# Kernel tuning notes

Measured on AMD Instinct MI355X. Metric: run time of the kernel, lower is better.

## Reference

```python
import jax, jax.numpy as jnp
import numpy as np
import math

B, SEQ_IN, D_IN = 4, 1028, 64
D = 1024          # hidden_size
H = 16            # num_heads
HD = D // H       # head_dim
L = 4             # num_layers
D_OUT = 1
EPS = 1e-6


def setup_inputs() -> dict:
    key = jax.random.key(0)
    ks = iter(jax.random.split(key, 32))
    s = 0.02
    inp = {}
    inp['x'] = jax.random.normal(next(ks), (B, SEQ_IN, D_IN), jnp.float32)
    # conv frontend (torch Conv1d weight layout: [out_ch, in_ch, k])
    inp['conv1_w'] = jax.random.normal(next(ks), (D // 2, D_IN, 3), jnp.float32) * s
    inp['conv1_b'] = jnp.zeros((D // 2,), jnp.float32)
    inp['conv2_w'] = jax.random.normal(next(ks), (D, D // 2, 3), jnp.float32) * s
    inp['conv2_b'] = jnp.zeros((D,), jnp.float32)
    # stacked per-layer params [L, ...]
    inp['lnA_w'] = jnp.ones((L, D), jnp.float32)
    inp['lnA_b'] = jnp.zeros((L, D), jnp.float32)
    inp['q_w'] = jax.random.normal(next(ks), (L, D, D), jnp.float32) * s
    inp['q_b'] = jnp.zeros((L, D), jnp.float32)
    inp['k_w'] = jax.random.normal(next(ks), (L, D, D), jnp.float32) * s
    inp['k_b'] = jnp.zeros((L, D), jnp.float32)
    inp['v_w'] = jax.random.normal(next(ks), (L, D, D), jnp.float32) * s
    inp['v_b'] = jnp.zeros((L, D), jnp.float32)
    inp['o_w'] = jax.random.normal(next(ks), (L, D, D), jnp.float32) * s
    inp['o_b'] = jnp.zeros((L, D), jnp.float32)
    inp['lnB_w'] = jnp.ones((L, D), jnp.float32)
    inp['lnB_b'] = jnp.zeros((L, D), jnp.float32)
    inp['f1_w'] = jax.random.normal(next(ks), (L, 2 * D, D), jnp.float32) * s
    inp['f1_b'] = jnp.zeros((L, 2 * D), jnp.float32)
    inp['f2_w'] = jax.random.normal(next(ks), (L, D, 2 * D), jnp.float32) * s
    inp['f2_b'] = jnp.zeros((L, D), jnp.float32)
    inp['fc_w'] = jax.random.normal(next(ks), (D_OUT, D), jnp.float32) * s
    inp['fc_b'] = jnp.zeros((D_OUT,), jnp.float32)
    return inp


def _layernorm(x, w, b):
    # torch-style: unbiased std (ddof=1), eps added to std (not var)
    mean = jnp.mean(x, axis=-1, keepdims=True)
    var = jnp.sum((x - mean) ** 2, axis=-1, keepdims=True) / (x.shape[-1] - 1)
    return w * ((x - mean) / (jnp.sqrt(var) + EPS)) + b


def _pos_encoding(S, d):
    pos = jnp.arange(S, dtype=jnp.float32)[:, None]
    div = jnp.exp(jnp.arange(0, d, 2, dtype=jnp.float32) * (-math.log(10000.0) / d))
    pe = jnp.zeros((S, d), jnp.float32)
    pe = pe.at[:, 0::2].set(jnp.sin(pos * div))
    pe = pe.at[:, 1::2].set(jnp.cos(pos * div))
    return pe


def _forward(x, conv1_w, conv1_b, conv2_w, conv2_b,
             lnA_w, lnA_b, q_w, q_b, k_w, k_b, v_w, v_b, o_w, o_b,
             lnB_w, lnB_b, f1_w, f1_b, f2_w, f2_b, fc_w, fc_b):
    dn = ('NCH', 'OIH', 'NCH')
    h = jnp.transpose(x, (0, 2, 1))                       # [B, D_in, S_in]
    h = jax.lax.conv_general_dilated(h, conv1_w, (1,), 'VALID', dimension_numbers=dn) + conv1_b[None, :, None]
    h = jax.lax.conv_general_dilated(h, conv2_w, (1,), 'VALID', dimension_numbers=dn) + conv2_b[None, :, None]
    h = jnp.transpose(h, (0, 2, 1))                       # [B, S, D]
    S = h.shape[1]
    h = h + _pos_encoding(S, D)[None]
    scale = 1.0 / math.sqrt(HD)

    def layer(xc, p):
        (lnaw, lnab, qw, qb, kw, kb, vw, vb, ow, ob,
         lnbw, lnbb, f1w, f1b, f2w, f2b) = p
        hn = _layernorm(xc, lnaw, lnab)
        q = (hn @ qw.T + qb).reshape(B, S, H, HD).transpose(0, 2, 1, 3)
        k = (hn @ kw.T + kb).reshape(B, S, H, HD).transpose(0, 2, 1, 3)
        v = (hn @ vw.T + vb).reshape(B, S, H, HD).transpose(0, 2, 1, 3)
        scores = jnp.einsum('bhsd,bhtd->bhst', q, k) * scale
        attn = scores / (1.0 + jnp.abs(scores))           # softsign, NOT softmax
        wv = jnp.einsum('bhst,bhtd->bhsd', attn, v)
        wv = wv.transpose(0, 2, 1, 3).reshape(B, S, D)
        xc = xc + (wv @ ow.T + ob)
        hn2 = _layernorm(xc, lnbw, lnbb)
        ff = jax.nn.relu(hn2 @ f1w.T + f1b) @ f2w.T + f2b
        return xc + ff, None

    params = (lnA_w, lnA_b, q_w, q_b, k_w, k_b, v_w, v_b, o_w, o_b,
              lnB_w, lnB_b, f1_w, f1_b, f2_w, f2_b)
    h, _ = jax.lax.scan(layer, h, params)
    pooled = jnp.mean(h, axis=1)                          # [B, D]
    return pooled @ fc_w.T + fc_b                         # [B, D_OUT]


def reference(x, conv1_w, conv1_b, conv2_w, conv2_b,
              lnA_w, lnA_b, q_w, q_b, k_w, k_b, v_w, v_b, o_w, o_b,
              lnB_w, lnB_b, f1_w, f1_b, f2_w, f2_b, fc_w, fc_b):
    return _forward(x, conv1_w, conv1_b, conv2_w, conv2_b,
                    lnA_w, lnA_b, q_w, q_b, k_w, k_b, v_w, v_b, o_w, o_b,
                    lnB_w, lnB_b, f1_w, f1_b, f2_w, f2_b, fc_w, fc_b)
```

## Files before the change

kernel.cpp:

```cpp
#include <hip/hip_runtime.h>
#include <hip/hip_bf16.h>
#include <math.h>

typedef __bf16 v8bf __attribute__((ext_vector_type(8)));
typedef float  v4f  __attribute__((ext_vector_type(4)));
typedef unsigned short v8us __attribute__((ext_vector_type(8)));

__device__ __forceinline__ unsigned short f2bfu(float f) {
    unsigned u = __builtin_bit_cast(unsigned, f);
    unsigned r = (u + 0x7fffu + ((u >> 16) & 1u)) >> 16;
    return (unsigned short)r;
}
__device__ __forceinline__ float bf2f(unsigned short u) {
    unsigned x = ((unsigned)u) << 16;
    return __builtin_bit_cast(float, x);
}

__device__ __forceinline__ long long swidx(int r, int k, int kt ) {
    return ((long long)((r >> 4) * kt + (k >> 5)) << 9)
         + (((k >> 3) & 3) << 7) + ((r & 15) << 3) + (k & 7);
}

#define GLDS16(g, s)                                                        \
    __builtin_amdgcn_global_load_lds(                                       \
        (const __attribute__((address_space(1))) void*)(g),                 \
        (__attribute__((address_space(3))) void*)(s), 16, 0, 0)

__global__ __launch_bounds__(256) void gemm_sw_k(
    const unsigned short* __restrict__ Asw,
    const unsigned short* __restrict__ Bsw,
    const float* __restrict__ bias,
    const float* __restrict__ res,
    float* __restrict__ Cf,
    unsigned short* __restrict__ Cb,
    unsigned short* __restrict__ Csw,
    unsigned short* __restrict__ Ct, int ctcol0,
    int M, int N, int K, int ldC, int relu)
{
    const int t = threadIdx.x;
    const int w = t >> 6;
    const int l = t & 63;

    int bx = blockIdx.x, by = blockIdx.y;
    {
        int nbx = gridDim.x;
        int nb  = nbx * gridDim.y;
        if ((nb & 7) == 0) {
            int bid = by * nbx + bx;
            int nid = (bid & 7) * (nb >> 3) + (bid >> 3);
            by = nid / nbx;
            bx = nid - by * nbx;
        }
    }
    const int m0 = by * 128;
    const int n0 = bx * 64;
    const int r16 = l & 15;
    const int qb  = l >> 4;
    const int wm = w >> 1, wn = w & 1;
    const int kt = K >> 5;

    const unsigned short* pa[4];
#pragma unroll
    for (int i = 0; i < 4; i++)
        pa[i] = Asw + ((long long)(((m0 >> 4) + 4 * wm + i) * kt) << 9) + l * 8;
    const unsigned short* pb[2];
#pragma unroll
    for (int j = 0; j < 2; j++)
        pb[j] = Bsw + ((long long)(((((n0 + 32 * wn) >> 4) + j)) * kt) << 9) + l * 8;

    v4f acc[4][2];
#pragma unroll
    for (int i = 0; i < 4; i++)
#pragma unroll
        for (int j = 0; j < 2; j++) acc[i][j] = (v4f){0.f, 0.f, 0.f, 0.f};

    v8bf Ab[4][4], Bb[4][2];

#pragma unroll
    for (int c = 0; c < 3; ++c) {
        const long long o = (long long)c << 9;
#pragma unroll
        for (int i = 0; i < 4; i++) Ab[c][i] = *(const v8bf*)(pa[i] + o);
#pragma unroll
        for (int j = 0; j < 2; j++) Bb[c][j] = *(const v8bf*)(pb[j] + o);
    }

    for (int s = 0; s < kt; s += 4) {
#pragma unroll
        for (int cc = 0; cc < 4; ++cc) {
            const int ring  = cc & 3;
            const int nring = (cc + 3) & 3;
            int nc = s + cc + 3;
            if (nc < kt) {
                const long long o = (long long)nc << 9;
#pragma unroll
                for (int i = 0; i < 4; i++)
                    Ab[nring][i] = *(const v8bf*)(pa[i] + o);
#pragma unroll
                for (int j = 0; j < 2; j++)
                    Bb[nring][j] = *(const v8bf*)(pb[j] + o);
            }
#pragma unroll
            for (int i = 0; i < 4; i++)
#pragma unroll
                for (int j = 0; j < 2; j++)
                    acc[i][j] = __builtin_amdgcn_mfma_f32_16x16x32_bf16(
                        Ab[ring][i], Bb[ring][j], acc[i][j], 0, 0, 0);
        }
    }

    float bv[2];
#pragma unroll
    for (int j = 0; j < 2; j++) bv[j] = bias[n0 + 32 * wn + 16 * j + r16];
    const int colbase = n0 + 32 * wn + r16;
    const int nt = N >> 5;
#pragma unroll
    for (int i = 0; i < 4; i++) {
        int rowb = m0 + 64 * wm + 16 * i + qb * 4;
#pragma unroll
        for (int j = 0; j < 2; j++) {
            int col = colbase + 16 * j;
            float v[4];
#pragma unroll
            for (int r = 0; r < 4; r++) v[r] = acc[i][j][r] + bv[j];
            if (Ct && col >= ctcol0) {
                ushort4 o;
                o.x = f2bfu(v[0]); o.y = f2bfu(v[1]);
                o.z = f2bfu(v[2]); o.w = f2bfu(v[3]);
                *(ushort4*)(Ct + ((long long)(rowb >> 10) << 20)
                            + (long long)(col - ctcol0) * 1024 + (rowb & 1023)) = o;
            } else if (Csw) {
#pragma unroll
                for (int r = 0; r < 4; r++) {
                    int row = rowb + r;
                    float vv = v[r];
                    if (relu) vv = fmaxf(vv, 0.f);
                    Csw[swidx(row, col, nt)] = f2bfu(vv);
                }
            } else {
#pragma unroll
                for (int r = 0; r < 4; r++) {
                    int row = rowb + r;
                    long long off = (long long)row * ldC + col;
                    float vv = v[r];
                    if (res)  vv += res[off];
                    if (relu) vv = fmaxf(vv, 0.f);
                    if (Cf) Cf[off] = vv;
                    if (Cb) ((unsigned short*)Cb)[off] = f2bfu(vv);
                }
            }
        }
    }
}

__global__ __launch_bounds__(256) void gemm_mfma_k(
    const __hip_bfloat16* __restrict__ A, int rpbA, long long bstrideA, int ldA,
    const __hip_bfloat16* __restrict__ B,
    const float* __restrict__ bias,
    const float* __restrict__ res,
    float* __restrict__ Cf,
    __hip_bfloat16* __restrict__ Cb,
    int M, int N, int K, int ldC, int relu)
{
    __shared__ __align__(16) __hip_bfloat16 As[2][8][64][8];
    __shared__ __align__(16) __hip_bfloat16 Bs[2][4][64][8];
    const int t  = threadIdx.x;
    const int w  = t >> 6;
    const int l  = t & 63;
    const int m0 = blockIdx.y * 128;
    const int n0 = blockIdx.x * 64;
    const int r16 = l & 15;
    const int qb  = l >> 4;
    const int wm = w >> 1, wn = w & 1;

    const __hip_bfloat16* gA[2];
#pragma unroll
    for (int tt = 0; tt < 2; tt++) {
        int arow = m0 + 16 * (2 * w + tt) + r16;
        gA[tt] = A + (long long)(arow / rpbA) * bstrideA
                   + (long long)(arow % rpbA) * ldA + qb * 8;
    }
    const __hip_bfloat16* gB = B + (long long)(n0 + 16 * w + r16) * K + qb * 8;

    v4f acc[4][2];
#pragma unroll
    for (int i = 0; i < 4; i++)
#pragma unroll
        for (int j = 0; j < 2; j++) acc[i][j] = (v4f){0.f, 0.f, 0.f, 0.f};

    GLDS16(gA[0], &As[0][2 * w + 0][0][0]);
    GLDS16(gA[1], &As[0][2 * w + 1][0][0]);
    GLDS16(gB,    &Bs[0][w][0][0]);
    __syncthreads();

    int cur = 0;
    for (int k0 = 32; k0 < K; k0 += 32) {
        v8bf af[4], bfr[2];
#pragma unroll
        for (int i = 0; i < 4; i++) af[i]  = *(const v8bf*)(&As[cur][4 * wm + i][l][0]);
#pragma unroll
        for (int j = 0; j < 2; j++) bfr[j] = *(const v8bf*)(&Bs[cur][2 * wn + j][l][0]);
        GLDS16(gA[0] + k0, &As[cur ^ 1][2 * w + 0][0][0]);
        GLDS16(gA[1] + k0, &As[cur ^ 1][2 * w + 1][0][0]);
        GLDS16(gB + k0,    &Bs[cur ^ 1][w][0][0]);
#pragma unroll
        for (int i = 0; i < 4; i++)
#pragma unroll
            for (int j = 0; j < 2; j++)
                acc[i][j] = __builtin_amdgcn_mfma_f32_16x16x32_bf16(
                    af[i], bfr[j], acc[i][j], 0, 0, 0);
        __syncthreads();
        cur ^= 1;
    }
    {
        v8bf af[4], bfr[2];
#pragma unroll
        for (int i = 0; i < 4; i++) af[i]  = *(const v8bf*)(&As[cur][4 * wm + i][l][0]);
#pragma unroll
        for (int j = 0; j < 2; j++) bfr[j] = *(const v8bf*)(&Bs[cur][2 * wn + j][l][0]);
#pragma unroll
        for (int i = 0; i < 4; i++)
#pragma unroll
            for (int j = 0; j < 2; j++)
                acc[i][j] = __builtin_amdgcn_mfma_f32_16x16x32_bf16(
                    af[i], bfr[j], acc[i][j], 0, 0, 0);
    }

    float bv[2];
#pragma unroll
    for (int j = 0; j < 2; j++) bv[j] = bias[n0 + 32 * wn + 16 * j + r16];
    const int colbase = n0 + 32 * wn + r16;
#pragma unroll
    for (int i = 0; i < 4; i++) {
        int rowb = m0 + 64 * wm + 16 * i + qb * 4;
#pragma unroll
        for (int j = 0; j < 2; j++) {
            int col = colbase + 16 * j;
#pragma unroll
            for (int r = 0; r < 4; r++) {
                int row = rowb + r;
                if (row >= M) continue;
                long long off = (long long)row * ldC + col;
                float vv = acc[i][j][r] + bv[j];
                if (res)  vv += res[off];
                if (relu) vv = fmaxf(vv, 0.f);
                if (Cf) Cf[off] = vv;
                if (Cb) ((unsigned short*)Cb)[off] = f2bfu(vv);
            }
        }
    }
}

__global__ __launch_bounds__(256) void attn_mfma_k(
    const unsigned short* __restrict__ QKV,
    const unsigned short* __restrict__ Vt,
    unsigned short* __restrict__ Osw)
{
    __shared__ __align__(16) unsigned short lds[25600];
    const int t = threadIdx.x, w = t >> 6, l = t & 63;
    const int bh = blockIdx.y, b = bh >> 4, h = bh & 15;
    const int s0 = blockIdx.x << 7;
    const int r16 = l & 15, q4 = l >> 4;
    const long long qrow0 = (long long)(b << 10) + s0;
    const int hoff = h << 6;

#pragma unroll
    for (int mi = 0; mi < 2; mi++)
#pragma unroll
        for (int kk = 0; kk < 2; kk++) {
            const unsigned short* g = QKV + (qrow0 + 32 * w + 16 * mi + r16) * 3072
                                      + hoff + 32 * kk + q4 * 8;
            GLDS16(g, &lds[(w * 4 + mi * 2 + kk) * 512]);
        }
    __syncthreads();
    v8bf qf[2][2];
#pragma unroll
    for (int mi = 0; mi < 2; mi++)
#pragma unroll
        for (int kk = 0; kk < 2; kk++)
            qf[mi][kk] = *(const v8bf*)&lds[(w * 4 + mi * 2 + kk) * 512 + l * 8];

    v4f oacc[2][4];
#pragma unroll
    for (int i = 0; i < 2; i++)
#pragma unroll
        for (int j = 0; j < 4; j++) oacc[i][j] = (v4f){0.f, 0.f, 0.f, 0.f};

    for (int t0 = 0; t0 < 1024; t0 += 64) {
#pragma unroll
        for (int rr = 0; rr < 2; rr++) {
            int r = 2 * w + rr, kk = r >> 2, j = r & 3;
            const unsigned short* gk = QKV
                + ((long long)(b << 10) + t0 + 16 * j + r16) * 3072
                + 1024 + hoff + 32 * kk + q4 * 8;
            GLDS16(gk, &lds[8192 + r * 512]);
            const unsigned short* gv = Vt + ((long long)b << 20)
                + (long long)(hoff + 16 * j + r16) * 1024 + t0 + 32 * kk + q4 * 8;
            GLDS16(gv, &lds[12288 + r * 512]);
        }
        __syncthreads();

        v8bf kf[2][4];
#pragma unroll
        for (int kk = 0; kk < 2; kk++)
#pragma unroll
            for (int j = 0; j < 4; j++)
                kf[kk][j] = *(const v8bf*)&lds[8192 + (kk * 4 + j) * 512 + l * 8];
        v4f sc[2][4];
#pragma unroll
        for (int i = 0; i < 2; i++)
#pragma unroll
            for (int j = 0; j < 4; j++) sc[i][j] = (v4f){0.f, 0.f, 0.f, 0.f};
#pragma unroll
        for (int kk = 0; kk < 2; kk++)
#pragma unroll
            for (int mi = 0; mi < 2; mi++)
#pragma unroll
                for (int j = 0; j < 4; j++)
                    sc[mi][j] = __builtin_amdgcn_mfma_f32_16x16x32_bf16(
                        qf[mi][kk], kf[kk][j], sc[mi][j], 0, 0, 0);

#pragma unroll
        for (int mi = 0; mi < 2; mi++)
#pragma unroll
            for (int j = 0; j < 4; j++)
#pragma unroll
                for (int r = 0; r < 4; r++) {
                    float v = sc[mi][j][r] * 0.125f;
                    float p = v * __builtin_amdgcn_rcpf(1.0f + fabsf(v));
                    lds[16384 + (32 * w + 16 * mi + q4 * 4 + r) * 72 + 16 * j + r16] = f2bfu(p);
                }

        v8bf pf[2][2], vf[2][4];
#pragma unroll
        for (int mi = 0; mi < 2; mi++)
#pragma unroll
            for (int kk = 0; kk < 2; kk++)
                pf[mi][kk] = *(const v8bf*)&lds[16384 + (32 * w + 16 * mi + r16) * 72
                                                + 32 * kk + q4 * 8];
#pragma unroll
        for (int kk = 0; kk < 2; kk++)
#pragma unroll
            for (int j = 0; j < 4; j++)
                vf[kk][j] = *(const v8bf*)&lds[12288 + (kk * 4 + j) * 512 + l * 8];
#pragma unroll
        for (int kk = 0; kk < 2; kk++)
#pragma unroll
            for (int mi = 0; mi < 2; mi++)
#pragma unroll
                for (int j = 0; j < 4; j++)
                    oacc[mi][j] = __builtin_amdgcn_mfma_f32_16x16x32_bf16(
                        pf[mi][kk], vf[kk][j], oacc[mi][j], 0, 0, 0);
        __syncthreads();
    }

#pragma unroll
    for (int mi = 0; mi < 2; mi++)
#pragma unroll
        for (int j = 0; j < 4; j++)
#pragma unroll
            for (int r = 0; r < 4; r++)
                lds[(32 * w + 16 * mi + q4 * 4 + r) * 72 + 16 * j + r16] =
                    f2bfu(oacc[mi][j][r]);
    __syncthreads();
    {
        int row = t >> 1, ch = (t & 1) << 5;
        int grow = (int)qrow0 + row;
#pragma unroll
        for (int i = 0; i < 4; i++) {
            int c0 = hoff + ch + 8 * i;
            v8us vv = *(const v8us*)&lds[row * 72 + ch + 8 * i];
            *(v8us*)(Osw + swidx(grow, c0, 32)) = vv;
        }
    }
}

__global__ __launch_bounds__(256) void layernorm_k(
    const float* __restrict__ x, const float* __restrict__ w,
    const float* __restrict__ b, unsigned short* __restrict__ ysw)
{
    int row = blockIdx.x;
    int t = threadIdx.x;
    float4 v = ((const float4*)(x + ((long long)row << 10)))[t];
    float s = v.x + v.y + v.z + v.w;
#pragma unroll
    for (int o = 32; o; o >>= 1) s += __shfl_down(s, o);
    __shared__ float red[4];
    __shared__ float red2[4];
    int wid = t >> 6, lane = t & 63;
    if (lane == 0) red[wid] = s;
    __syncthreads();
    float mean = (red[0] + red[1] + red[2] + red[3]) * (1.0f / 1024.0f);
    float dx = v.x - mean, dy = v.y - mean, dz = v.z - mean, dw = v.w - mean;
    float sq = dx * dx + dy * dy + dz * dz + dw * dw;
#pragma unroll
    for (int o = 32; o; o >>= 1) sq += __shfl_down(sq, o);
    if (lane == 0) red2[wid] = sq;
    __syncthreads();
    float var = (red2[0] + red2[1] + red2[2] + red2[3]) * (1.0f / 1023.0f);
    float inv = 1.0f / (sqrtf(var) + 1e-6f);
    float4 W  = ((const float4*)w)[t];
    float4 Bv = ((const float4*)b)[t];
    ushort4 o;
    o.x = f2bfu(W.x * (dx * inv) + Bv.x);
    o.y = f2bfu(W.y * (dy * inv) + Bv.y);
    o.z = f2bfu(W.z * (dz * inv) + Bv.z);
    o.w = f2bfu(W.w * (dw * inv) + Bv.w);
    int c0 = t << 2;
    *(ushort4*)(ysw + swidx(row, c0, 32)) = o;
}

__global__ __launch_bounds__(256) void add_pos_k(float* __restrict__ h)
{
    int idx = blockIdx.x * 256 + threadIdx.x;
    int d = idx & 1023;
    int s = (idx >> 10) & 1023;
    int e = d & ~1;
    float div = expf(-9.210340371976184f * (float)e * (1.0f / 1024.0f));
    float arg = (float)s * div;
    float pe = (d & 1) ? cosf(arg) : sinf(arg);
    h[idx] += pe;
}

__global__ __launch_bounds__(256) void convert_k(
    const float* __restrict__ src, unsigned short* __restrict__ dst, int n4)
{
    int i = blockIdx.x * 256 + threadIdx.x;
    if (i >= n4) return;
    float4 v = ((const float4*)src)[i];
    ushort4 o;
    o.x = f2bfu(v.x); o.y = f2bfu(v.y); o.z = f2bfu(v.z); o.w = f2bfu(v.w);
    ((ushort4*)dst)[i] = o;
}

__global__ __launch_bounds__(256) void convert_layer_sw_k(
    const float* __restrict__ q, const float* __restrict__ k,
    const float* __restrict__ v, const float* __restrict__ o,
    const float* __restrict__ f1, const float* __restrict__ f2,
    unsigned short* __restrict__ dst)
{
    int idx = blockIdx.x * 256 + threadIdx.x;
    const float* src;
    unsigned short* db;
    int Ksh, rf;
    if (idx < 0x100000) {
        int region = idx >> 18;
        rf = idx & 0x3FFFF;
        src = (region == 0) ? q : (region == 1) ? k : (region == 2) ? v : o;
        db = dst + ((long long)region << 20);
        Ksh = 10;
    } else if (idx < 0x180000) {
        rf = idx - 0x100000; src = f1; db = dst + (4LL << 20); Ksh = 10;
    } else {
        rf = idx - 0x180000; src = f2; db = dst + (6LL << 20); Ksh = 11;
    }
    float4 vv = ((const float4*)src)[rf];
    int flatf = rf << 2;
    int n  = flatf >> Ksh;
    int k0 = flatf & ((1 << Ksh) - 1);
    ushort4 ov;
    ov.x = f2bfu(vv.x); ov.y = f2bfu(vv.y); ov.z = f2bfu(vv.z); ov.w = f2bfu(vv.w);
    *(ushort4*)(db + swidx(n, k0, 1 << (Ksh - 5))) = ov;
}

__global__ __launch_bounds__(256) void concat3_k(
    const float* __restrict__ a, const float* __restrict__ b,
    const float* __restrict__ c, float* __restrict__ o)
{
    int i = blockIdx.x * 256 + threadIdx.x;
    o[i] = (i < 1024) ? a[i] : ((i < 2048) ? b[i - 1024] : c[i - 2048]);
}

__global__ __launch_bounds__(256) void reorder_w_k(
    const float* __restrict__ src, unsigned short* __restrict__ dst, int OC, int IC)
{
    int idx = blockIdx.x * 256 + threadIdx.x;
    if (idx >= OC * IC * 3) return;
    int k  = idx % 3;
    int ic = (idx / 3) % IC;
    int oc = idx / (3 * IC);
    dst[(oc * 3 + k) * IC + ic] = f2bfu(src[idx]);
}

__global__ __launch_bounds__(256) void meanpool_part_k(
    const float* __restrict__ h, float* __restrict__ part)
{
    int g = blockIdx.x;
    int b = g >> 6, rblk = g & 63;
    const float4* base = (const float4*)(h + ((long long)b << 20)
                                           + ((long long)(rblk * 16) << 10));
    float4 s = {0.f, 0.f, 0.f, 0.f};
#pragma unroll
    for (int i = 0; i < 16; i++) {
        float4 v = base[i * 256 + threadIdx.x];
        s.x += v.x; s.y += v.y; s.z += v.z; s.w += v.w;
    }
    ((float4*)part)[g * 256 + threadIdx.x] = s;
}

__global__ __launch_bounds__(256) void meanpool_red_k(
    const float* __restrict__ part, float* __restrict__ pooled)
{
    int idx = blockIdx.x * 256 + threadIdx.x;
    int b = idx >> 10, d = idx & 1023;
    const float* p = part + ((long long)(b * 64) << 10) + d;
    float s = 0.f;
#pragma unroll 8
    for (int r = 0; r < 64; r++) s += p[r << 10];
    pooled[idx] = s * (1.0f / 1024.0f);
}

__global__ __launch_bounds__(256) void fc_k(
    const float* __restrict__ p, const float* __restrict__ w,
    const float* __restrict__ fb, float* __restrict__ out)
{
    int b = blockIdx.x, t = threadIdx.x;
    float s = 0.f;
    for (int i = t; i < 1024; i += 256) s += p[(b << 10) + i] * w[i];
#pragma unroll
    for (int o = 32; o; o >>= 1) s += __shfl_down(s, o);
    __shared__ float red[4];
    if ((t & 63) == 0) red[t >> 6] = s;
    __syncthreads();
    if (t == 0) out[b] = red[0] + red[1] + red[2] + red[3] + fb[0];
}

extern "C" void kernel_launch(void* const* d_in, const int* in_sizes, int n_in,
                              void* d_out, int out_size, void* d_ws, size_t ws_size,
                              hipStream_t stream)
{
    const float* x    = (const float*)d_in[0];
    const float* c1w  = (const float*)d_in[1];
    const float* c1b  = (const float*)d_in[2];
    const float* c2w  = (const float*)d_in[3];
    const float* c2b  = (const float*)d_in[4];
    const float* lnAw = (const float*)d_in[5];
    const float* lnAb = (const float*)d_in[6];
    const float* qw   = (const float*)d_in[7];
    const float* qbi  = (const float*)d_in[8];
    const float* kw   = (const float*)d_in[9];
    const float* kbi  = (const float*)d_in[10];
    const float* vw   = (const float*)d_in[11];
    const float* vbi  = (const float*)d_in[12];
    const float* ow   = (const float*)d_in[13];
    const float* obi  = (const float*)d_in[14];
    const float* lnBw = (const float*)d_in[15];
    const float* lnBb = (const float*)d_in[16];
    const float* f1w  = (const float*)d_in[17];
    const float* f1b  = (const float*)d_in[18];
    const float* f2w  = (const float*)d_in[19];
    const float* f2b  = (const float*)d_in[20];
    const float* fcw  = (const float*)d_in[21];
    const float* fcb  = (const float*)d_in[22];
    float* out = (float*)d_out;

    float* ws = (float*)d_ws;
    typedef __hip_bfloat16 bf;
    typedef unsigned short us;
    float* h    = ws;
    us* hn_b    = (us*)(ws + 4194304);
    us* qkv_b   = (us*)(ws + 6291456);
    us* ff_b    = qkv_b;
    us* wq_b    = (us*)(ws + 12582912);
    us* wo_b    = (us*)(ws + 14155776);
    us* wf1_b   = (us*)(ws + 14680064);
    us* wf2_b   = (us*)(ws + 15728640);
    us* xb      = (us*)(ws + 16777216);
    us* h1b     = (us*)(ws + 16912896);
    us* w1t_b   = (us*)(ws + 17963520);
    us* w2t_b   = (us*)(ws + 18012672);
    float* pooled = ws + 18799104;
    us* Vt      = (us*)(ws + 18803200);
    float* bqkv = ws + 20900352;
    float* mp_part = ws + 20903424;

    convert_k<<<dim3(257), 256, 0, stream>>>(x, xb, 65792);
    reorder_w_k<<<dim3(384),  256, 0, stream>>>(c1w, w1t_b, 512, 64);
    reorder_w_k<<<dim3(6144), 256, 0, stream>>>(c2w, w2t_b, 1024, 512);

    gemm_mfma_k<<<dim3(8, 33), 256, 0, stream>>>(
        (const bf*)xb, 1026, 1028LL * 64, 64, (const bf*)w1t_b,
        c1b, nullptr, nullptr, (bf*)h1b, 4104, 512, 192, 512, 0);
    gemm_mfma_k<<<dim3(16, 32), 256, 0, stream>>>(
        (const bf*)h1b, 1024, 1026LL * 512, 512, (const bf*)w2t_b,
        c2b, nullptr, h, nullptr, 4096, 1024, 1536, 1024, 0);
    add_pos_k<<<dim3(16384), 256, 0, stream>>>(h);

    for (int l = 0; l < 4; l++) {
        long long wo  = (long long)l * 1048576;
        long long wo2 = (long long)l * 2097152;
        convert_layer_sw_k<<<dim3(8192), 256, 0, stream>>>(
            qw + wo, kw + wo, vw + wo, ow + wo, f1w + wo2, f2w + wo2, wq_b);
        concat3_k<<<dim3(12), 256, 0, stream>>>(qbi + l * 1024, kbi + l * 1024,
                                                vbi + l * 1024, bqkv);

        layernorm_k<<<dim3(4096), 256, 0, stream>>>(h, lnAw + l * 1024, lnAb + l * 1024, hn_b);
        gemm_sw_k<<<dim3(48, 32), 256, 0, stream>>>(
            hn_b, wq_b, bqkv, nullptr, nullptr, qkv_b, nullptr, Vt, 2048,
            4096, 3072, 1024, 3072, 0);
        attn_mfma_k<<<dim3(8, 64), 256, 0, stream>>>(qkv_b, Vt, hn_b);
        gemm_sw_k<<<dim3(16, 32), 256, 0, stream>>>(
            hn_b, wo_b, obi + l * 1024, h, h, nullptr, nullptr, nullptr, 0,
            4096, 1024, 1024, 1024, 0);
        layernorm_k<<<dim3(4096), 256, 0, stream>>>(h, lnBw + l * 1024, lnBb + l * 1024, hn_b);
        gemm_sw_k<<<dim3(32, 32), 256, 0, stream>>>(
            hn_b, wf1_b, f1b + l * 2048, nullptr, nullptr, nullptr, ff_b, nullptr, 0,
            4096, 2048, 1024, 2048, 1);
        gemm_sw_k<<<dim3(16, 32), 256, 0, stream>>>(
            ff_b, wf2_b, f2b + l * 1024, h, h, nullptr, nullptr, nullptr, 0,
            4096, 1024, 2048, 1024, 0);
    }

    meanpool_part_k<<<dim3(256), 256, 0, stream>>>(h, mp_part);
    meanpool_red_k<<<dim3(16), 256, 0, stream>>>(mp_part, pooled);
    fc_k<<<dim3(4), 256, 0, stream>>>(pooled, fcw, fcb, out);
}
```

Measured before the change: 1.151 ms.

## Stage GEMM operands through double-buffered LDS and widen tile to 128x128

The swizzled-layout GEMM no longer has each wave load its A/B fragments straight from global memory into a register ring. Operands are now staged into double-buffered shared memory with global_load_lds, and the block tile grows from 128x64 to 128x128, so each wave computes a 64x64 sub-tile (4x4 MFMAs). The aim is to cut redundant global traffic, since waves now share A/B fragments through LDS. The cost is a __syncthreads per k-step, more accumulator registers, and half as many blocks per launch. Grid sizes for the four per-layer GEMMs are halved to match.

```diff
diff --git a/kernel.cpp b/kernel.cpp
--- a/kernel.cpp
+++ b/kernel.cpp
@@ -37,6 +37,8 @@
     unsigned short* __restrict__ Ct, int ctcol0,
     int M, int N, int K, int ldC, int relu)
 {
+    __shared__ __align__(16) unsigned short As[2][8][512];
+    __shared__ __align__(16) unsigned short Bs[2][8][512];
     const int t = threadIdx.x;
     const int w = t >> 6;
     const int l = t & 63;
@@ -53,72 +55,74 @@
         }
     }
     const int m0 = by * 128;
-    const int n0 = bx * 64;
+    const int n0 = bx * 128;
     const int r16 = l & 15;
     const int qb  = l >> 4;
     const int wm = w >> 1, wn = w & 1;
     const int kt = K >> 5;
 
-    const unsigned short* pa[4];
+    const unsigned short* gA0 = Asw + (((long long)((m0 >> 4) + 2 * w) * kt) << 9) + l * 8;
+    const unsigned short* gA1 = gA0 + ((long long)kt << 9);
+    const unsigned short* gB0 = Bsw + (((long long)((n0 >> 4) + 2 * w) * kt) << 9) + l * 8;
+    const unsigned short* gB1 = gB0 + ((long long)kt << 9);
+
+    v4f acc[4][4];
 #pragma unroll
     for (int i = 0; i < 4; i++)
-        pa[i] = Asw + ((long long)(((m0 >> 4) + 4 * wm + i) * kt) << 9) + l * 8;
-    const unsigned short* pb[2];
-#pragma unroll
-    for (int j = 0; j < 2; j++)
-        pb[j] = Bsw + ((long long)(((((n0 + 32 * wn) >> 4) + j)) * kt) << 9) + l * 8;
-
-    v4f acc[4][2];
-#pragma unroll
-    for (int i = 0; i < 4; i++)
-#pragma unroll
-        for (int j = 0; j < 2; j++) acc[i][j] = (v4f){0.f, 0.f, 0.f, 0.f};
-
-    v8bf Ab[4][4], Bb[4][2];
-
-#pragma unroll
-    for (int c = 0; c < 3; ++c) {
+#pragma unroll
+        for (int j = 0; j < 4; j++) acc[i][j] = (v4f){0.f, 0.f, 0.f, 0.f};
+
+    GLDS16(gA0, &As[0][2 * w + 0][0]);
+    GLDS16(gA1, &As[0][2 * w + 1][0]);
+    GLDS16(gB0, &Bs[0][2 * w + 0][0]);
+    GLDS16(gB1, &Bs[0][2 * w + 1][0]);
+    __syncthreads();
+
+    int cur = 0;
+    for (int c = 1; c < kt; c++) {
         const long long o = (long long)c << 9;
-#pragma unroll
-        for (int i = 0; i < 4; i++) Ab[c][i] = *(const v8bf*)(pa[i] + o);
-#pragma unroll
-        for (int j = 0; j < 2; j++) Bb[c][j] = *(const v8bf*)(pb[j] + o);
-    }
-
-    for (int s = 0; s < kt; s += 4) {
-#pragma unroll
-        for (int cc = 0; cc < 4; ++cc) {
-            const int ring  = cc & 3;
-            const int nring = (cc + 3) & 3;
-            int nc = s + cc + 3;
-            if (nc < kt) {
-                const long long o = (long long)nc << 9;
-#pragma unroll
-                for (int i = 0; i < 4; i++)
-                    Ab[nring][i] = *(const v8bf*)(pa[i] + o);
-#pragma unroll
-                for (int j = 0; j < 2; j++)
-                    Bb[nring][j] = *(const v8bf*)(pb[j] + o);
-            }
-#pragma unroll
-            for (int i = 0; i < 4; i++)
-#pragma unroll
-                for (int j = 0; j < 2; j++)
-                    acc[i][j] = __builtin_amdgcn_mfma_f32_16x16x32_bf16(
-                        Ab[ring][i], Bb[ring][j], acc[i][j], 0, 0, 0);
-        }
-    }
-
-    float bv[2];
-#pragma unroll
-    for (int j = 0; j < 2; j++) bv[j] = bias[n0 + 32 * wn + 16 * j + r16];
-    const int colbase = n0 + 32 * wn + r16;
+        GLDS16(gA0 + o, &As[cur ^ 1][2 * w + 0][0]);
+        GLDS16(gA1 + o, &As[cur ^ 1][2 * w + 1][0]);
+        GLDS16(gB0 + o, &Bs[cur ^ 1][2 * w + 0][0]);
+        GLDS16(gB1 + o, &Bs[cur ^ 1][2 * w + 1][0]);
+        v8bf af[4], bfr[4];
+#pragma unroll
+        for (int i = 0; i < 4; i++) af[i]  = *(const v8bf*)(&As[cur][4 * wm + i][l * 8]);
+#pragma unroll
+        for (int j = 0; j < 4; j++) bfr[j] = *(const v8bf*)(&Bs[cur][4 * wn + j][l * 8]);
+#pragma unroll
+        for (int i = 0; i < 4; i++)
+#pragma unroll
+            for (int j = 0; j < 4; j++)
+                acc[i][j] = __builtin_amdgcn_mfma_f32_16x16x32_bf16(
+                    af[i], bfr[j], acc[i][j], 0, 0, 0);
+        __syncthreads();
+        cur ^= 1;
+    }
+    {
+        v8bf af[4], bfr[4];
+#pragma unroll
+        for (int i = 0; i < 4; i++) af[i]  = *(const v8bf*)(&As[cur][4 * wm + i][l * 8]);
+#pragma unroll
+        for (int j = 0; j < 4; j++) bfr[j] = *(const v8bf*)(&Bs[cur][4 * wn + j][l * 8]);
+#pragma unroll
+        for (int i = 0; i < 4; i++)
+#pragma unroll
+            for (int j = 0; j < 4; j++)
+                acc[i][j] = __builtin_amdgcn_mfma_f32_16x16x32_bf16(
+                    af[i], bfr[j], acc[i][j], 0, 0, 0);
+    }
+
+    float bv[4];
+#pragma unroll
+    for (int j = 0; j < 4; j++) bv[j] = bias[n0 + 64 * wn + 16 * j + r16];
+    const int colbase = n0 + 64 * wn + r16;
     const int nt = N >> 5;
 #pragma unroll
     for (int i = 0; i < 4; i++) {
         int rowb = m0 + 64 * wm + 16 * i + qb * 4;
 #pragma unroll
-        for (int j = 0; j < 2; j++) {
+        for (int j = 0; j < 4; j++) {
             int col = colbase + 16 * j;
             float v[4];
 #pragma unroll
@@ -595,18 +599,18 @@
                                                 vbi + l * 1024, bqkv);
 
         layernorm_k<<<dim3(4096), 256, 0, stream>>>(h, lnAw + l * 1024, lnAb + l * 1024, hn_b);
-        gemm_sw_k<<<dim3(48, 32), 256, 0, stream>>>(
+        gemm_sw_k<<<dim3(24, 32), 256, 0, stream>>>(
             hn_b, wq_b, bqkv, nullptr, nullptr, qkv_b, nullptr, Vt, 2048,
             4096, 3072, 1024, 3072, 0);
         attn_mfma_k<<<dim3(8, 64), 256, 0, stream>>>(qkv_b, Vt, hn_b);
-        gemm_sw_k<<<dim3(16, 32), 256, 0, stream>>>(
+        gemm_sw_k<<<dim3(8, 32), 256, 0, stream>>>(
             hn_b, wo_b, obi + l * 1024, h, h, nullptr, nullptr, nullptr, 0,
             4096, 1024, 1024, 1024, 0);
         layernorm_k<<<dim3(4096), 256, 0, stream>>>(h, lnBw + l * 1024, lnBb + l * 1024, hn_b);
-        gemm_sw_k<<<dim3(32, 32), 256, 0, stream>>>(
+        gemm_sw_k<<<dim3(16, 32), 256, 0, stream>>>(
             hn_b, wf1_b, f1b + l * 2048, nullptr, nullptr, nullptr, ff_b, nullptr, 0,
             4096, 2048, 1024, 2048, 1);
-        gemm_sw_k<<<dim3(16, 32), 256, 0, stream>>>(
+        gemm_sw_k<<<dim3(8, 32), 256, 0, stream>>>(
             ff_b, wf2_b, f2b + l * 1024, h, h, nullptr, nullptr, nullptr, 0,
             4096, 1024, 2048, 1024, 0);
     }
```

After: 1.279 ms. 11.1% more time.
